# Performance work log

Hardware: AMD Instinct MI355X
Metric: run time of the kernel (lower is better)

## Reference

```python
import jax, jax.numpy as jnp
import numpy as np

SHIFT = 7  # shift_size; pad = 3


def _gn(x, w, b, eps=1e-5):
    # GroupNorm(1, C): normalize over (C,H,W) per sample, affine per channel
    m = jnp.mean(x, axis=(1, 2, 3), keepdims=True)
    v = jnp.var(x, axis=(1, 2, 3), keepdims=True)
    return (x - m) * jax.lax.rsqrt(v + eps) * w[None, :, None, None] + b[None, :, None, None]


def _conv1x1(x, w, b):
    return jnp.einsum('bchw,oc->bohw', x, w) + b[None, :, None, None]


def _gelu(x):
    return jax.nn.gelu(x, approximate=False)


def _shift_h(x, size):
    # CUDA kernel semantics: g = c // ceil(C/size); s = -(g - size//2);
    # out[n,c,h,w] = x[n,c,h+s,w] if in-bounds else 0  (dim=2)
    B, C, H, W = x.shape
    pad = size // 2
    group = -(-C // size)  # ceil
    s = pad - (jnp.arange(C) // group)              # [C], values in [-pad, pad]
    xp = jnp.pad(x, ((0, 0), (0, 0), (pad, pad), (0, 0)))
    idx = jnp.arange(H)[None, :] + s[:, None] + pad  # [C,H], in [0, H+2p-1]
    c = jnp.arange(C)[:, None]
    return xp[:, c, idx, :]


def _shift_w(x, size):
    return _shift_h(x.swapaxes(2, 3), size).swapaxes(2, 3)


def _axial_shift(x, c1w, c1b, n1w, n1b, c21w, c21b, c22w, c22b, n2w, n2b, c3w, c3b):
    x = _gelu(_gn(_conv1x1(x, c1w, c1b), n1w, n1b))
    x_lr = _shift_w(x, SHIFT)
    x_td = _shift_h(x, SHIFT)
    x_lr = _gelu(_conv1x1(x_lr, c21w, c21b))
    x_td = _gelu(_conv1x1(x_td, c22w, c22b))
    x = _gn(x_lr + x_td, n2w, n2b)
    return _conv1x1(x, c3w, c3b)


def setup_inputs() -> dict:
    B, C, H, W = 16, 256, 56, 56
    HID = 4 * C
    key = jax.random.key(0)
    ks = jax.random.split(key, 8)
    wscale = 0.05
    inp = {
        'x': jax.random.normal(ks[0], (B, C, H, W), jnp.float32),
        'n1_w': jnp.ones((C,), jnp.float32), 'n1_b': jnp.zeros((C,), jnp.float32),
        'as_c1_w': jax.random.normal(ks[1], (C, C), jnp.float32) * wscale,
        'as_c1_b': jnp.zeros((C,), jnp.float32),
        'as_n1_w': jnp.ones((C,), jnp.float32), 'as_n1_b': jnp.zeros((C,), jnp.float32),
        'as_c21_w': jax.random.normal(ks[2], (C, C), jnp.float32) * wscale,
        'as_c21_b': jnp.zeros((C,), jnp.float32),
        'as_c22_w': jax.random.normal(ks[3], (C, C), jnp.float32) * wscale,
        'as_c22_b': jnp.zeros((C,), jnp.float32),
        'as_n2_w': jnp.ones((C,), jnp.float32), 'as_n2_b': jnp.zeros((C,), jnp.float32),
        'as_c3_w': jax.random.normal(ks[4], (C, C), jnp.float32) * wscale,
        'as_c3_b': jnp.zeros((C,), jnp.float32),
        'n2_w': jnp.ones((C,), jnp.float32), 'n2_b': jnp.zeros((C,), jnp.float32),
        'fc1_w': jax.random.normal(ks[5], (HID, C), jnp.float32) * wscale,
        'fc1_b': jnp.zeros((HID,), jnp.float32),
        'fc2_w': jax.random.normal(ks[6], (C, HID), jnp.float32) * wscale,
        'fc2_b': jnp.zeros((C,), jnp.float32),
    }
    return inp


def reference(x, n1_w, n1_b, as_c1_w, as_c1_b, as_n1_w, as_n1_b,
              as_c21_w, as_c21_b, as_c22_w, as_c22_b, as_n2_w, as_n2_b,
              as_c3_w, as_c3_b, n2_w, n2_b, fc1_w, fc1_b, fc2_w, fc2_b):
    # AxialShiftedBlock: x = x + AxialShift(norm1(x)); x = x + Mlp(norm2(x))
    h = _gn(x, n1_w, n1_b)
    h = _axial_shift(h, as_c1_w, as_c1_b, as_n1_w, as_n1_b,
                     as_c21_w, as_c21_b, as_c22_w, as_c22_b,
                     as_n2_w, as_n2_b, as_c3_w, as_c3_b)
    x = x + h
    h = _gn(x, n2_w, n2_b)
    h = _gelu(_conv1x1(h, fc1_w, fc1_b))
    h = _conv1x1(h, fc2_w, fc2_b)
    return x + h
```

## Files before the change

kernel.cpp:

```cpp
#include <hip/hip_runtime.h>

typedef __attribute__((ext_vector_type(4))) float f32x4;
typedef __attribute__((ext_vector_type(8))) short bf16x8;
typedef __attribute__((ext_vector_type(4))) unsigned short u16x4;
typedef unsigned short u16;

#define HW 3136
#define NSEG 49
#define NELF 802816.0f
#define EPS 1e-5f

__device__ __forceinline__ short f2bf(float f) {
  union { float f; unsigned u; } v; v.f = f;
  unsigned r = (v.u + 0x7FFFu + ((v.u >> 16) & 1u)) >> 16;
  return (short)r;
}
__device__ __forceinline__ float b2f(u16 u) {
  union { unsigned u; float f; } v; v.u = ((unsigned)u) << 16;
  return v.f;
}
__device__ __forceinline__ float fgelu(float x) {
  float x2 = x * x;
  float u = x * (0.7978845608f + 0.0356774081f * x2);
  float e = __expf(-2.0f * u);
// ... 90 lines not shown
  red[t] = s; red[256 + t] = q;
  __syncthreads();
  for (int off = 128; off > 0; off >>= 1) {
    if (t < off) { red[t] += red[t + off]; red[256 + t] += red[256 + t + off]; }
    __syncthreads();
  }
  if (t == 0) { atomicAdd(&st[n * 2], red[0]); atomicAdd(&st[n * 2 + 1], red[256]); }
}

__global__ void e2_kernel(const u16* __restrict__ y, u16* __restrict__ tb,
                          const float* __restrict__ gw, const float* __restrict__ gb,
                          const float* __restrict__ stats) {
  const size_t NG = (size_t)16 * HW * 32;
  for (size_t g = (size_t)blockIdx.x * blockDim.x + threadIdx.x; g < NG;
       g += (size_t)gridDim.x * blockDim.x) {
    size_t base = g * 8;
    int n = (int)(base / 802816);
    int c0 = (int)(base & 255);
    float sm = stats[n * 2], sq = stats[n * 2 + 1];
    float mn = sm * (1.0f / NELF);
    float rstd = rsqrtf(sq * (1.0f / NELF) - mn * mn + EPS);
    bf16x8 v = *(const bf16x8*)(y + base);
    bf16x8 o;
#pragma unroll
    for (int j = 0; j < 8; ++j) {
      float sc = rstd * gw[c0 + j];
      float sh = gb[c0 + j] - mn * sc;
      o[j] = f2bf(fgelu(b2f((u16)v[j]) * sc + sh));
    }
    *(bf16x8*)(tb + base) = o;
  }
}

#define STG(bsel, ks_) do {                                                              \
    const int k0_ = (ks_) * 32;                                                          \
    if (PRO == 0) {                                                                      \
      gload16(srcB0 + k0_, &lds[16384 + (bsel) * 2048 + wave * 512]);                    \
    } else {                                                                             \
      int c0_ = k0_ + segB * 8;                                                          \
      int g0_ = c0_ / 37;                                                                \
      int js_ = (g0_ + 1) * 37 - c0_;                                                    \
      int s0_ = 3 - g0_;                                                                 \
      if (js_ >= 8) {                                                                    \
        if ((unsigned)(wpB + s0_) < 56u) {                                               \
          int dp_ = (PRO == 1) ? s0_ : 56 * s0_;                                         \
          gload16(actT + (nHW + pB + dp_) * KTOT + segB * 8 + k0_,                       \
                  &lds[16384 + (bsel) * 2048 + wave * 512]);                             \
        } else {                                                                         \
          bf16x8 zz = {0, 0, 0, 0, 0, 0, 0, 0};                                          \
          *(bf16x8*)&lds[16384 + (bsel) * 2048 + t * 8] = zz;                            \
        }                                                                                \
      } else {                                                                           \
        bf16x8 vv;                                                                       \
        _Pragma("unroll") for (int j = 0; j < 8; ++j) {                                  \
          int s_ = s0_ - (j >= js_ ? 1 : 0);                                             \
          int dp_ = (PRO == 1) ? s_ : 56 * s_;                                           \
          int pp_ = pB + dp_; pp_ = pp_ < 0 ? 0 : (pp_ > HW - 1 ? HW - 1 : pp_);         \
          u16 uv = actT[(nHW + pp_) * KTOT + c0_ + j];                                   \
          vv[j] = ((unsigned)(wpB + s_) < 56u) ? (short)uv : (short)0;                   \
        }                                                                                \
        *(bf16x8*)&lds[16384 + (bsel) * 2048 + t * 8] = vv;                              \
      }                                                                                  \
    }                                                                                    \
    gload16(sA0 + k0_, &lds[(bsel) * 8192 + wave * 512]);                                \
    gload16(sA1 + k0_, &lds[(bsel) * 8192 + 2048 + wave * 512]);                         \
    gload16(sA2 + k0_, &lds[(bsel) * 8192 + 4096 + wave * 512]);                         \
    gload16(sA3 + k0_, &lds[(bsel) * 8192 + 6144 + wave * 512]);                         \
  } while (0)

template<int KTOT, int OTOT, int PRO, int EPI>
__global__ __launch_bounds__(256, 3) void gemmS(
    const u16* __restrict__ actT, const u16* __restrict__ wt,
    const float* __restrict__ Sg, const float* __restrict__ Sb,
    const float* __restrict__ stats_in, float* __restrict__ stats_out,
    const u16* __restrict__ residCL, float* __restrict__ out_f32,
    u16* __restrict__ outT)
{
  constexpr int NK = KTOT / 32;
  constexpr bool FOLD = (EPI == 0 || EPI == 1 || EPI == 2);
  __shared__ __align__(16) u16 lds[20480];
  const int t = threadIdx.x;
  const int lane = t & 63, wave = t >> 6;
  const int fr = lane & 15, fq = lane >> 4;
  const int n = blockIdx.x / NSEG;
  const int hw0 = (blockIdx.x % NSEG) * 64;
  const int obase_blk = blockIdx.y * 256;
  const size_t nHW = (size_t)n * HW;

  const int rB = t >> 2;
  const int segB = ((t & 3) - (rB >> 1)) & 3;
  const int pB = hw0 + rB;
  int wpB = 0;
  if (PRO == 1) wpB = pB % 56;
  if (PRO == 2) wpB = pB / 56;
  const u16* srcB0 = actT + (nHW + pB) * KTOT + segB * 8;
  const u16 *sA0, *sA1, *sA2, *sA3;
  {
    int u, r, sg;
    u = t;       r = u >> 2; sg = ((u & 3) - (r >> 1)) & 3; sA0 = wt + (size_t)(obase_blk + r) * KTOT + sg * 8;
    u = t + 256; r = u >> 2; sg = ((u & 3) - (r >> 1)) & 3; sA1 = wt + (size_t)(obase_blk + r) * KTOT + sg * 8;
    u = t + 512; r = u >> 2; sg = ((u & 3) - (r >> 1)) & 3; sA2 = wt + (size_t)(obase_blk + r) * KTOT + sg * 8;
    u = t + 768; r = u >> 2; sg = ((u & 3) - (r >> 1)) & 3; sA3 = wt + (size_t)(obase_blk + r) * KTOT + sg * 8;
  }

  int aU[4], bU[4];
#pragma unroll
  for (int os = 0; os < 4; ++os) { int row = wave * 64 + os * 16 + fr; aU[os] = (4 * row + ((fq + (row >> 1)) & 3)) * 8; }
#pragma unroll
  for (int ps = 0; ps < 4; ++ps) { int row = ps * 16 + fr;             bU[ps] = (4 * row + ((fq + (row >> 1)) & 3)) * 8; }

  float mr = 0.f, rstd = 1.f;
  if (FOLD) {
    float sm = stats_in[n * 2], sq = stats_in[n * 2 + 1];
    float mn = sm * (1.0f / NELF);
    rstd = rsqrtf(sq * (1.0f / NELF) - mn * mn + EPS);
    mr = mn * rstd;
  }

  f32x4 acc[4][4];
#pragma unroll
  for (int a = 0; a < 4; ++a)
#pragma unroll
    for (int b = 0; b < 4; ++b) acc[a][b] = (f32x4){0.f, 0.f, 0.f, 0.f};

  STG(0, 0);
  __syncthreads();
#pragma unroll
  for (int ks = 0; ks < NK; ++ks) {
    const int b = ks & 1;
    if (ks + 1 < NK) STG(b ^ 1, ks + 1);
    bf16x8 afr[4], bfr[4];
#pragma unroll
    for (int os = 0; os < 4; ++os) afr[os] = *(const bf16x8*)&lds[b * 8192 + aU[os]];
#pragma unroll
    for (int ps = 0; ps < 4; ++ps) bfr[ps] = *(const bf16x8*)&lds[16384 + b * 2048 + bU[ps]];
#pragma unroll
    for (int os = 0; os < 4; ++os)
#pragma unroll
      for (int ps = 0; ps < 4; ++ps)
        acc[os][ps] = __builtin_amdgcn_mfma_f32_16x16x32_bf16(afr[os], bfr[ps], acc[os][ps], 0, 0, 0);
    __syncthreads();
  }

  float lsum = 0.f, lsq = 0.f;
  if (EPI != 3) {
#pragma unroll
    for (int os = 0; os < 4; ++os) {
      const int ob = obase_blk + wave * 64 + os * 16 + fq * 4;
      float be[4];
      if (FOLD) {
        float4 g4 = *(const float4*)&Sg[ob];
        float4 s4 = *(const float4*)&Sb[ob];
        be[0] = s4.x - mr * g4.x; be[1] = s4.y - mr * g4.y;
        be[2] = s4.z - mr * g4.z; be[3] = s4.w - mr * g4.w;
      } else {
        float4 s4 = *(const float4*)&Sb[ob];
        be[0] = s4.x; be[1] = s4.y; be[2] = s4.z; be[3] = s4.w;
      }
#pragma unroll
      for (int ps = 0; ps < 4; ++ps) {
        const int pix = ps * 16 + fr;
        u16x4 rv = {0, 0, 0, 0};
        if (EPI == 1 || EPI == 5)
          rv = *(const u16x4*)&residCL[(nHW + hw0 + pix) * 256 + ob];
        u16x4 pk;
#pragma unroll
        for (int j = 0; j < 4; ++j) {
          float v = FOLD ? fmaf(acc[os][ps][j], rstd, be[j]) : (acc[os][ps][j] + be[j]);
          if (EPI == 2 || EPI == 4 || EPI == 5) v = fgelu(v);
          if (EPI == 1 || EPI == 5) v += b2f(rv[j]);
          if (EPI == 0 || EPI == 1 || EPI == 5) { lsum += v; lsq += v * v; }
          pk[j] = (u16)f2bf(v);
        }
        const int qd = wave * 16 + os * 4 + fq;
        const int uq = qd ^ ((pix & 15) << 2);
        *(u16x4*)((char*)lds + pix * 512 + uq * 8) = pk;
      }
    }
    __syncthreads();
    {
      const int p2 = t >> 2;
#pragma unroll
      for (int r = 0; r < 8; ++r) {
        const int oct = (t & 3) + (r << 2);
        const int up = (2 * oct) ^ ((p2 & 15) << 2);
        bf16x8 v = *(const bf16x8*)((char*)lds + p2 * 512 + up * 8);
        *(bf16x8*)&outT[(nHW + hw0 + p2) * OTOT + obase_blk + oct * 8] = v;
      }
    }
  } else {
#pragma unroll
    for (int os = 0; os < 4; ++os) {
      const int ob = wave * 64 + os * 16 + fq * 4;
      float4 b4 = *(const float4*)&Sb[ob];
      float bb[4] = {b4.x, b4.y, b4.z, b4.w};
#pragma unroll
      for (int ps = 0; ps < 4; ++ps) {
        const int pix = ps * 16 + fr;
        u16x4 rv = *(const u16x4*)&residCL[(nHW + hw0 + pix) * 256 + ob];
#pragma unroll
        for (int j = 0; j < 4; ++j)
          out_f32[((size_t)n * 256 + ob + j) * HW + hw0 + pix] = acc[os][ps][j] + bb[j] + b2f(rv[j]);
      }
    }
  }

  if (EPI == 0 || EPI == 1 || EPI == 5) {
    __syncthreads();
    float* red = (float*)lds;
    red[t] = lsum; red[256 + t] = lsq;
    __syncthreads();
    for (int off = 128; off > 0; off >>= 1) {
      if (t < off) { red[t] += red[t + off]; red[256 + t] += red[256 + t + off]; }
      __syncthreads();
    }
    if (t == 0) { atomicAdd(&stats_out[n * 2], red[0]); atomicAdd(&stats_out[n * 2 + 1], red[256]); }
  }
}

extern "C" void kernel_launch(void* const* d_in, const int* in_sizes, int n_in,
                              void* d_out, int out_size, void* d_ws, size_t ws_size,
                              hipStream_t stream) {
  const float* x     = (const float*)d_in[0];
  const float* n1_w  = (const float*)d_in[1];
  const float* n1_b  = (const float*)d_in[2];
  const float* c1_w  = (const float*)d_in[3];
  const float* c1_b  = (const float*)d_in[4];
  const float* an1_w = (const float*)d_in[5];
  const float* an1_b = (const float*)d_in[6];
  const float* c21_w = (const float*)d_in[7];
  const float* c21_b = (const float*)d_in[8];
  const float* c22_w = (const float*)d_in[9];
  const float* c22_b = (const float*)d_in[10];
  const float* an2_w = (const float*)d_in[11];
  const float* an2_b = (const float*)d_in[12];
  const float* c3_w  = (const float*)d_in[13];
  const float* c3_b  = (const float*)d_in[14];
  const float* n2_w  = (const float*)d_in[15];
  const float* n2_b  = (const float*)d_in[16];
  const float* fc1_w = (const float*)d_in[17];
  const float* fc1_b = (const float*)d_in[18];
  const float* fc2_w = (const float*)d_in[19];
  const float* fc2_b = (const float*)d_in[20];

  char* ws = (char*)d_ws;
  float* stats = (float*)ws;
  float* sums  = (float*)(ws + 1024);
  u16* wbuf = (u16*)(ws + 16384);
  u16* wb_c1g  = wbuf;
  u16* wb_c21  = wbuf + 65536;
  u16* wb_c22  = wbuf + 131072;
  u16* wb_c3g  = wbuf + 196608;
  u16* wb_fc1g = wbuf + 262144;
  u16* wb_fc2  = wbuf + 524288;
  const size_t AB = 25690112;
  char* A0 = ws + 1638400;
  u16* xT  = (u16*)(A0);
  u16* yT  = (u16*)(A0 + AB);
  u16* tT  = (u16*)(A0 + 2 * AB);
  u16* zA  = (u16*)(A0 + 3 * AB);
  u16* zT  = (u16*)(A0 + AB);
  u16* x2T = (u16*)(A0 + 4 * AB);
  u16* hid = (u16*)(A0);
  float* out = (float*)d_out;

  hipMemsetAsync(stats, 0, 512, stream);
  wfold_kernel<<<768, 256, 0, stream>>>(c1_w, c21_w, c22_w, c3_w, fc1_w, fc2_w,
                                        n1_w, an2_w, n2_w, wbuf);
  rowsum_kernel<<<6, 256, 0, stream>>>(c1_w, c1_b, n1_w, n1_b, c3_w, c3_b, an2_w, an2_b,
                                       fc1_w, fc1_b, n2_w, n2_b, sums);
  t0_kernel<<<784, 256, 0, stream>>>(x, xT, stats + 0);
  gemmS<256, 256, 0, 0><<<dim3(784, 1), 256, 0, stream>>>(
      xT, wb_c1g, sums, sums + 256, stats + 0, stats + 32, nullptr, nullptr, yT);
  e2_kernel<<<2048, 256, 0, stream>>>(yT, tT, an1_w, an1_b, stats + 32);
  gemmS<256, 256, 1, 4><<<dim3(784, 1), 256, 0, stream>>>(
      tT, wb_c21, nullptr, c21_b, nullptr, nullptr, nullptr, nullptr, zA);
  gemmS<256, 256, 2, 5><<<dim3(784, 1), 256, 0, stream>>>(
      tT, wb_c22, nullptr, c22_b, nullptr, stats + 64, zA, nullptr, zT);
  gemmS<256, 256, 0, 1><<<dim3(784, 1), 256, 0, stream>>>(
      zT, wb_c3g, sums + 512, sums + 768, stats + 64, stats + 96, xT, nullptr, x2T);
  gemmS<256, 1024, 0, 2><<<dim3(784, 4), 256, 0, stream>>>(
      x2T, wb_fc1g, sums + 1024, sums + 2048, stats + 96, nullptr, nullptr, nullptr, hid);
  gemmS<1024, 256, 0, 3><<<dim3(784, 1), 256, 0, stream>>>(
      hid, wb_fc2, nullptr, fc2_b, nullptr, nullptr, x2T, out, nullptr);
}
```

Measured before the change: 317.1 us.

## Retile GEMMs to 256x224 blocks with full-weight LDS residency and 8 waves

```diff
diff --git a/kernel.cpp b/kernel.cpp
--- a/kernel.cpp
+++ b/kernel.cpp
@@ -146,83 +146,124 @@
   }
 }
 
-#define STG(bsel, ks_) do {                                                              \
-    const int k0_ = (ks_) * 32;                                                          \
-    if (PRO == 0) {                                                                      \
-      gload16(srcB0 + k0_, &lds[16384 + (bsel) * 2048 + wave * 512]);                    \
-    } else {                                                                             \
-      int c0_ = k0_ + segB * 8;                                                          \
-      int g0_ = c0_ / 37;                                                                \
-      int js_ = (g0_ + 1) * 37 - c0_;                                                    \
-      int s0_ = 3 - g0_;                                                                 \
-      if (js_ >= 8) {                                                                    \
-        if ((unsigned)(wpB + s0_) < 56u) {                                               \
-          int dp_ = (PRO == 1) ? s0_ : 56 * s0_;                                         \
-          gload16(actT + (nHW + pB + dp_) * KTOT + segB * 8 + k0_,                       \
-                  &lds[16384 + (bsel) * 2048 + wave * 512]);                             \
-        } else {                                                                         \
-          bf16x8 zz = {0, 0, 0, 0, 0, 0, 0, 0};                                          \
-          *(bf16x8*)&lds[16384 + (bsel) * 2048 + t * 8] = zz;                            \
-        }                                                                                \
-      } else {                                                                           \
-        bf16x8 vv;                                                                       \
-        _Pragma("unroll") for (int j = 0; j < 8; ++j) {                                  \
-          int s_ = s0_ - (j >= js_ ? 1 : 0);                                             \
-          int dp_ = (PRO == 1) ? s_ : 56 * s_;                                           \
-          int pp_ = pB + dp_; pp_ = pp_ < 0 ? 0 : (pp_ > HW - 1 ? HW - 1 : pp_);         \
-          u16 uv = actT[(nHW + pp_) * KTOT + c0_ + j];                                   \
-          vv[j] = ((unsigned)(wpB + s_) < 56u) ? (short)uv : (short)0;                   \
-        }                                                                                \
-        *(bf16x8*)&lds[16384 + (bsel) * 2048 + t * 8] = vv;                              \
-      }                                                                                  \
-    }                                                                                    \
-    gload16(sA0 + k0_, &lds[(bsel) * 8192 + wave * 512]);                                \
-    gload16(sA1 + k0_, &lds[(bsel) * 8192 + 2048 + wave * 512]);                         \
-    gload16(sA2 + k0_, &lds[(bsel) * 8192 + 4096 + wave * 512]);                         \
-    gload16(sA3 + k0_, &lds[(bsel) * 8192 + 6144 + wave * 512]);                         \
-  } while (0)
-
-template<int KTOT, int OTOT, int PRO, int EPI>
-__global__ __launch_bounds__(256, 3) void gemmS(
+template<int PRO, int EPI, int OTOT>
+__global__ __launch_bounds__(512, 2) void gemmW(
     const u16* __restrict__ actT, const u16* __restrict__ wt,
     const float* __restrict__ Sg, const float* __restrict__ Sb,
     const float* __restrict__ stats_in, float* __restrict__ stats_out,
-    const u16* __restrict__ residCL, float* __restrict__ out_f32,
-    u16* __restrict__ outT)
+    const u16* __restrict__ residCL, u16* __restrict__ outT)
 {
-  constexpr int NK = KTOT / 32;
   constexpr bool FOLD = (EPI == 0 || EPI == 1 || EPI == 2);
-  __shared__ __align__(16) u16 lds[20480];
+  __shared__ __align__(16) u16 lds[72704];
   const int t = threadIdx.x;
   const int lane = t & 63, wave = t >> 6;
   const int fr = lane & 15, fq = lane >> 4;
-  const int n = blockIdx.x / NSEG;
-  const int hw0 = (blockIdx.x % NSEG) * 64;
-  const int obase_blk = blockIdx.y * 256;
+  const int wo = wave >> 1, wp = wave & 1;
+  const int n = blockIdx.x / 14;
+  const int hw0 = (blockIdx.x % 14) * 224;
+  const int obase = blockIdx.y << 8;
   const size_t nHW = (size_t)n * HW;
 
-  const int rB = t >> 2;
-  const int segB = ((t & 3) - (rB >> 1)) & 3;
-  const int pB = hw0 + rB;
-  int wpB = 0;
-  if (PRO == 1) wpB = pB % 56;
-  if (PRO == 2) wpB = pB / 56;
-  const u16* srcB0 = actT + (nHW + pB) * KTOT + segB * 8;
-  const u16 *sA0, *sA1, *sA2, *sA3;
   {
-    int u, r, sg;
-    u = t;       r = u >> 2; sg = ((u & 3) - (r >> 1)) & 3; sA0 = wt + (size_t)(obase_blk + r) * KTOT + sg * 8;
-    u = t + 256; r = u >> 2; sg = ((u & 3) - (r >> 1)) & 3; sA1 = wt + (size_t)(obase_blk + r) * KTOT + sg * 8;
-    u = t + 512; r = u >> 2; sg = ((u & 3) - (r >> 1)) & 3; sA2 = wt + (size_t)(obase_blk + r) * KTOT + sg * 8;
-    u = t + 768; r = u >> 2; sg = ((u & 3) - (r >> 1)) & 3; sA3 = wt + (size_t)(obase_blk + r) * KTOT + sg * 8;
-  }
-
-  int aU[4], bU[4];
-#pragma unroll
-  for (int os = 0; os < 4; ++os) { int row = wave * 64 + os * 16 + fr; aU[os] = (4 * row + ((fq + (row >> 1)) & 3)) * 8; }
-#pragma unroll
-  for (int ps = 0; ps < 4; ++ps) { int row = ps * 16 + fr;             bU[ps] = (4 * row + ((fq + (row >> 1)) & 3)) * 8; }
-
+    int u0 = t, u1 = t + 512;
+    int r0 = u0 >> 2, sg0 = ((u0 & 3) - (r0 >> 1)) & 3;
+    int r1 = u1 >> 2, sg1 = ((u1 & 3) - (r1 >> 1)) & 3;
+    const u16* w0 = wt + (size_t)(obase + r0) * 256 + sg0 * 8;
+    const u16* w1 = wt + (size_t)(obase + r1) * 256 + sg1 * 8;
+#pragma unroll
+    for (int k = 0; k < 8; ++k) {
+      gload16(w0 + k * 32, &lds[k * 8192 + wave * 512]);
+      gload16(w1 + k * 32, &lds[k * 8192 + 4096 + wave * 512]);
+    }
+  }
+
+  const bool bact = (t < 448);
+  const int brow = t >> 1;
+  const int bp = hw0 + brow;
+  int bwp = 0;
+  if (PRO == 1) bwp = bp % 56;
+  if (PRO == 2) bwp = bp / 56;
+  const int bj0 = (t & 1) * 2;
+  const u16* bsrc = actT + (nHW + bp) * 256;
+
+  auto loadBu = [&](int c0, bf16x8& v) {
+    if (PRO == 0) {
+      v = *(const bf16x8*)(bsrc + c0);
+    } else {
+      int g0 = c0 / 37;
+      int js = (g0 + 1) * 37 - c0;
+      int s0 = 3 - g0;
+      if (js >= 8) {
+        if ((unsigned)(bwp + s0) < 56u) {
+          int dp = (PRO == 1) ? s0 : 56 * s0;
+          v = *(const bf16x8*)(bsrc + dp * 256 + c0);
+        } else {
+          v = (bf16x8){0, 0, 0, 0, 0, 0, 0, 0};
+        }
+      } else {
+#pragma unroll
+        for (int j = 0; j < 8; ++j) {
+          int s = s0 - (j >= js ? 1 : 0);
+          int dp = (PRO == 1) ? s : 56 * s;
+          int pp = bp + dp; pp = pp < 0 ? 0 : (pp > HW - 1 ? HW - 1 : pp);
+          u16 uv = actT[(nHW + pp) * 256 + c0 + j];
+          v[j] = ((unsigned)(bwp + s) < 56u) ? (short)uv : (short)0;
+        }
+      }
+    }
+  };
+
+  int aU[4], bO[7];
+#pragma unroll
+  for (int os = 0; os < 4; ++os) { int row = wo * 64 + os * 16 + fr; aU[os] = (4 * row + ((fq + (row >> 1)) & 3)) * 8; }
+#pragma unroll
+  for (int ps = 0; ps < 7; ++ps) bO[ps] = 65536 + (fq * 224 + wp * 112 + ps * 16 + fr) * 8;
+
+  f32x4 acc[4][7];
+#pragma unroll
+  for (int a = 0; a < 4; ++a)
+#pragma unroll
+    for (int b = 0; b < 7; ++b) acc[a][b] = (f32x4){0.f, 0.f, 0.f, 0.f};
+
+  {
+    bf16x8 v0, v1;
+    if (bact) { loadBu(bj0 * 8, v0); loadBu(bj0 * 8 + 8, v1); }
+    asm volatile("s_waitcnt vmcnt(0)" ::: "memory");
+    if (bact) {
+      *(bf16x8*)&lds[65536 + (bj0 * 224 + brow) * 8] = v0;
+      *(bf16x8*)&lds[65536 + ((bj0 + 1) * 224 + brow) * 8] = v1;
+    }
+  }
+  __syncthreads();
+
+#pragma unroll
+  for (int k = 0; k < 8; ++k) {
+    bf16x8 n0, n1;
+    if (k < 7 && bact) { loadBu((k + 1) * 32 + bj0 * 8, n0); loadBu((k + 1) * 32 + bj0 * 8 + 8, n1); }
+    bf16x8 afr[4], bfr[7];
+#pragma unroll
+    for (int os = 0; os < 4; ++os) afr[os] = *(const bf16x8*)&lds[k * 8192 + aU[os]];
+#pragma unroll
+    for (int ps = 0; ps < 7; ++ps) bfr[ps] = *(const bf16x8*)&lds[bO[ps]];
+#pragma unroll
+    for (int os = 0; os < 4; ++os)
+#pragma unroll
+      for (int ps = 0; ps < 7; ++ps)
+        acc[os][ps] = __builtin_amdgcn_mfma_f32_16x16x32_bf16(afr[os], bfr[ps], acc[os][ps], 0, 0, 0);
+    __builtin_amdgcn_s_barrier();
+    if (k < 7) {
+      if (bact) {
+        *(bf16x8*)&lds[65536 + (bj0 * 224 + brow) * 8] = n0;
+        *(bf16x8*)&lds[65536 + ((bj0 + 1) * 224 + brow) * 8] = n1;
+      }
+      asm volatile("s_waitcnt lgkmcnt(0)" ::: "memory");
+      __builtin_amdgcn_sched_barrier(0);
+      __builtin_amdgcn_s_barrier();
+    }
+  }
+  __syncthreads();
+
+  char* tl = (char*)lds;
   float mr = 0.f, rstd = 1.f;
   if (FOLD) {
     float sm = stats_in[n * 2], sq = stats_in[n * 2 + 1];
@@ -230,105 +271,138 @@
     rstd = rsqrtf(sq * (1.0f / NELF) - mn * mn + EPS);
     mr = mn * rstd;
   }
-
-  f32x4 acc[4][4];
-#pragma unroll
-  for (int a = 0; a < 4; ++a)
-#pragma unroll
-    for (int b = 0; b < 4; ++b) acc[a][b] = (f32x4){0.f, 0.f, 0.f, 0.f};
-
-  STG(0, 0);
-  __syncthreads();
-#pragma unroll
-  for (int ks = 0; ks < NK; ++ks) {
-    const int b = ks & 1;
-    if (ks + 1 < NK) STG(b ^ 1, ks + 1);
-    bf16x8 afr[4], bfr[4];
-#pragma unroll
-    for (int os = 0; os < 4; ++os) afr[os] = *(const bf16x8*)&lds[b * 8192 + aU[os]];
-#pragma unroll
-    for (int ps = 0; ps < 4; ++ps) bfr[ps] = *(const bf16x8*)&lds[16384 + b * 2048 + bU[ps]];
-#pragma unroll
-    for (int os = 0; os < 4; ++os)
-#pragma unroll
-      for (int ps = 0; ps < 4; ++ps)
-        acc[os][ps] = __builtin_amdgcn_mfma_f32_16x16x32_bf16(afr[os], bfr[ps], acc[os][ps], 0, 0, 0);
-    __syncthreads();
-  }
-
   float lsum = 0.f, lsq = 0.f;
-  if (EPI != 3) {
-#pragma unroll
-    for (int os = 0; os < 4; ++os) {
-      const int ob = obase_blk + wave * 64 + os * 16 + fq * 4;
-      float be[4];
-      if (FOLD) {
-        float4 g4 = *(const float4*)&Sg[ob];
-        float4 s4 = *(const float4*)&Sb[ob];
-        be[0] = s4.x - mr * g4.x; be[1] = s4.y - mr * g4.y;
-        be[2] = s4.z - mr * g4.z; be[3] = s4.w - mr * g4.w;
-      } else {
-        float4 s4 = *(const float4*)&Sb[ob];
-        be[0] = s4.x; be[1] = s4.y; be[2] = s4.z; be[3] = s4.w;
+#pragma unroll
+  for (int os = 0; os < 4; ++os) {
+    const int obl = wo * 64 + os * 16 + fq * 4;
+    const int ob = obase + obl;
+    float be[4];
+    if (FOLD) {
+      float4 g4 = *(const float4*)&Sg[ob];
+      float4 s4 = *(const float4*)&Sb[ob];
+      be[0] = s4.x - mr * g4.x; be[1] = s4.y - mr * g4.y;
+      be[2] = s4.z - mr * g4.z; be[3] = s4.w - mr * g4.w;
+    } else {
+      float4 s4 = *(const float4*)&Sb[obl];
+      be[0] = s4.x; be[1] = s4.y; be[2] = s4.z; be[3] = s4.w;
+    }
+#pragma unroll
+    for (int ps = 0; ps < 7; ++ps) {
+      const int pix = wp * 112 + ps * 16 + fr;
+      u16x4 rv = {0, 0, 0, 0};
+      if (EPI == 1 || EPI == 5)
+        rv = *(const u16x4*)&residCL[(nHW + hw0 + pix) * 256 + obl];
+      u16x4 pk;
+#pragma unroll
+      for (int j = 0; j < 4; ++j) {
+        float v = FOLD ? fmaf(acc[os][ps][j], rstd, be[j]) : (acc[os][ps][j] + be[j]);
+        if (EPI == 2 || EPI == 4 || EPI == 5) v = fgelu(v);
+        if (EPI == 1 || EPI == 5) v += b2f(rv[j]);
+        if (EPI == 0 || EPI == 1 || EPI == 5) { lsum += v; lsq += v * v; }
+        pk[j] = (u16)f2bf(v);
       }
-#pragma unroll
-      for (int ps = 0; ps < 4; ++ps) {
-        const int pix = ps * 16 + fr;
-        u16x4 rv = {0, 0, 0, 0};
-        if (EPI == 1 || EPI == 5)
-          rv = *(const u16x4*)&residCL[(nHW + hw0 + pix) * 256 + ob];
-        u16x4 pk;
-#pragma unroll
-        for (int j = 0; j < 4; ++j) {
-          float v = FOLD ? fmaf(acc[os][ps][j], rstd, be[j]) : (acc[os][ps][j] + be[j]);
-          if (EPI == 2 || EPI == 4 || EPI == 5) v = fgelu(v);
-          if (EPI == 1 || EPI == 5) v += b2f(rv[j]);
-          if (EPI == 0 || EPI == 1 || EPI == 5) { lsum += v; lsq += v * v; }
-          pk[j] = (u16)f2bf(v);
-        }
-        const int qd = wave * 16 + os * 4 + fq;
-        const int uq = qd ^ ((pix & 15) << 2);
-        *(u16x4*)((char*)lds + pix * 512 + uq * 8) = pk;
-      }
-    }
-    __syncthreads();
-    {
-      const int p2 = t >> 2;
-#pragma unroll
-      for (int r = 0; r < 8; ++r) {
-        const int oct = (t & 3) + (r << 2);
-        const int up = (2 * oct) ^ ((p2 & 15) << 2);
-        bf16x8 v = *(const bf16x8*)((char*)lds + p2 * 512 + up * 8);
-        *(bf16x8*)&outT[(nHW + hw0 + p2) * OTOT + obase_blk + oct * 8] = v;
-      }
-    }
-  } else {
-#pragma unroll
-    for (int os = 0; os < 4; ++os) {
-      const int ob = wave * 64 + os * 16 + fq * 4;
-      float4 b4 = *(const float4*)&Sb[ob];
-      float bb[4] = {b4.x, b4.y, b4.z, b4.w};
-#pragma unroll
-      for (int ps = 0; ps < 4; ++ps) {
-        const int pix = ps * 16 + fr;
-        u16x4 rv = *(const u16x4*)&residCL[(nHW + hw0 + pix) * 256 + ob];
-#pragma unroll
-        for (int j = 0; j < 4; ++j)
-          out_f32[((size_t)n * 256 + ob + j) * HW + hw0 + pix] = acc[os][ps][j] + bb[j] + b2f(rv[j]);
-      }
-    }
+      const int qd = wo * 16 + os * 4 + fq;
+      const int uq = qd ^ ((pix & 15) << 2);
+      *(u16x4*)(tl + pix * 512 + uq * 8) = pk;
+    }
+  }
+  __syncthreads();
+#pragma unroll
+  for (int r = 0; r < 14; ++r) {
+    int idx = t + r * 512;
+    int pix = idx >> 5, oct = idx & 31;
+    int up = (2 * oct) ^ ((pix & 15) << 2);
+    bf16x8 v = *(const bf16x8*)(tl + pix * 512 + up * 8);
+    *(bf16x8*)&outT[(nHW + hw0 + pix) * OTOT + obase + oct * 8] = v;
   }
 
   if (EPI == 0 || EPI == 1 || EPI == 5) {
     __syncthreads();
     float* red = (float*)lds;
-    red[t] = lsum; red[256 + t] = lsq;
+    red[t] = lsum; red[512 + t] = lsq;
     __syncthreads();
-    for (int off = 128; off > 0; off >>= 1) {
-      if (t < off) { red[t] += red[t + off]; red[256 + t] += red[256 + t + off]; }
+    for (int off = 256; off > 0; off >>= 1) {
+      if (t < off) { red[t] += red[t + off]; red[512 + t] += red[512 + t + off]; }
       __syncthreads();
     }
-    if (t == 0) { atomicAdd(&stats_out[n * 2], red[0]); atomicAdd(&stats_out[n * 2 + 1], red[256]); }
+    if (t == 0) { atomicAdd(&stats_out[n * 2], red[0]); atomicAdd(&stats_out[n * 2 + 1], red[512]); }
+  }
+}
+
+__global__ __launch_bounds__(512, 2) void gemmF(
+    const u16* __restrict__ hidT, const u16* __restrict__ wt,
+    const float* __restrict__ bias, const u16* __restrict__ residCL,
+    float* __restrict__ out_f32)
+{
+  __shared__ __align__(16) u16 lds[30720];
+  const int t = threadIdx.x;
+  const int lane = t & 63, wave = t >> 6;
+  const int fr = lane & 15, fq = lane >> 4;
+  const int wo = wave >> 1, wp = wave & 1;
+  const int n = blockIdx.x / 14;
+  const int hw0 = (blockIdx.x % 14) * 224;
+  const size_t nHW = (size_t)n * HW;
+
+  int u0 = t, u1 = t + 512;
+  int r0 = u0 >> 2, sg0 = ((u0 & 3) - (r0 >> 1)) & 3;
+  int r1 = u1 >> 2, sg1 = ((u1 & 3) - (r1 >> 1)) & 3;
+  const u16* wA0 = wt + (size_t)r0 * 1024 + sg0 * 8;
+  const u16* wA1 = wt + (size_t)r1 * 1024 + sg1 * 8;
+  const int c1 = (2 * wave) % 14, c2 = (2 * wave + 1) % 14;
+  const int ub1 = c1 * 64 + lane, ub2 = c2 * 64 + lane;
+  const u16* hb1 = hidT + (nHW + hw0 + ub1 % 224) * 1024 + (ub1 / 224) * 8;
+  const u16* hb2 = hidT + (nHW + hw0 + ub2 % 224) * 1024 + (ub2 / 224) * 8;
+
+  auto stgf = [&](int bs, int k0) {
+    gload16(wA0 + k0, &lds[bs * 8192 + wave * 512]);
+    gload16(wA1 + k0, &lds[bs * 8192 + 4096 + wave * 512]);
+    gload16(hb1 + k0, &lds[16384 + bs * 7168 + c1 * 512]);
+    gload16(hb2 + k0, &lds[16384 + bs * 7168 + c2 * 512]);
+  };
+
+  int aU[4], bO[7];
+#pragma unroll
+  for (int os = 0; os < 4; ++os) { int row = wo * 64 + os * 16 + fr; aU[os] = (4 * row + ((fq + (row >> 1)) & 3)) * 8; }
+#pragma unroll
+  for (int ps = 0; ps < 7; ++ps) bO[ps] = 16384 + (fq * 224 + wp * 112 + ps * 16 + fr) * 8;
+
+  f32x4 acc[4][7];
+#pragma unroll
+  for (int a = 0; a < 4; ++a)
+#pragma unroll
+    for (int b = 0; b < 7; ++b) acc[a][b] = (f32x4){0.f, 0.f, 0.f, 0.f};
+
+  stgf(0, 0);
+  __syncthreads();
+  for (int ks = 0; ks < 32; ++ks) {
+    const int bs = ks & 1;
+    if (ks < 31) stgf(bs ^ 1, (ks + 1) * 32);
+    bf16x8 afr[4], bfr[7];
+#pragma unroll
+    for (int os = 0; os < 4; ++os) afr[os] = *(const bf16x8*)&lds[bs * 8192 + aU[os]];
+#pragma unroll
+    for (int ps = 0; ps < 7; ++ps) bfr[ps] = *(const bf16x8*)&lds[bs * 7168 + bO[ps]];
+#pragma unroll
+    for (int os = 0; os < 4; ++os)
+#pragma unroll
+      for (int ps = 0; ps < 7; ++ps)
+        acc[os][ps] = __builtin_amdgcn_mfma_f32_16x16x32_bf16(afr[os], bfr[ps], acc[os][ps], 0, 0, 0);
+    __syncthreads();
+  }
+
+#pragma unroll
+  for (int os = 0; os < 4; ++os) {
+    const int ob = wo * 64 + os * 16 + fq * 4;
+    float4 b4 = *(const float4*)&bias[ob];
+    float bb[4] = {b4.x, b4.y, b4.z, b4.w};
+#pragma unroll
+    for (int ps = 0; ps < 7; ++ps) {
+      const int pix = wp * 112 + ps * 16 + fr;
+      u16x4 rv = *(const u16x4*)&residCL[(nHW + hw0 + pix) * 256 + ob];
+#pragma unroll
+      for (int j = 0; j < 4; ++j)
+        out_f32[((size_t)n * 256 + ob + j) * HW + hw0 + pix] = acc[os][ps][j] + bb[j] + b2f(rv[j]);
+    }
   }
 }
 
@@ -384,17 +458,16 @@
   rowsum_kernel<<<6, 256, 0, stream>>>(c1_w, c1_b, n1_w, n1_b, c3_w, c3_b, an2_w, an2_b,
                                        fc1_w, fc1_b, n2_w, n2_b, sums);
   t0_kernel<<<784, 256, 0, stream>>>(x, xT, stats + 0);
-  gemmS<256, 256, 0, 0><<<dim3(784, 1), 256, 0, stream>>>(
-      xT, wb_c1g, sums, sums + 256, stats + 0, stats + 32, nullptr, nullptr, yT);
+  gemmW<0, 0, 256><<<dim3(224, 1), 512, 0, stream>>>(
+      xT, wb_c1g, sums, sums + 256, stats + 0, stats + 32, nullptr, yT);
   e2_kernel<<<2048, 256, 0, stream>>>(yT, tT, an1_w, an1_b, stats + 32);
-  gemmS<256, 256, 1, 4><<<dim3(784, 1), 256, 0, stream>>>(
-      tT, wb_c21, nullptr, c21_b, nullptr, nullptr, nullptr, nullptr, zA);
-  gemmS<256, 256, 2, 5><<<dim3(784, 1), 256, 0, stream>>>(
-      tT, wb_c22, nullptr, c22_b, nullptr, stats + 64, zA, nullptr, zT);
-  gemmS<256, 256, 0, 1><<<dim3(784, 1), 256, 0, stream>>>(
-      zT, wb_c3g, sums + 512, sums + 768, stats + 64, stats + 96, xT, nullptr, x2T);
-  gemmS<256, 1024, 0, 2><<<dim3(784, 4), 256, 0, stream>>>(
-      x2T, wb_fc1g, sums + 1024, sums + 2048, stats + 96, nullptr, nullptr, nullptr, hid);
-  gemmS<1024, 256, 0, 3><<<dim3(784, 1), 256, 0, stream>>>(
-      hid, wb_fc2, nullptr, fc2_b, nullptr, nullptr, x2T, out, nullptr);
-}
+  gemmW<1, 4, 256><<<dim3(224, 1), 512, 0, stream>>>(
+      tT, wb_c21, nullptr, c21_b, nullptr, nullptr, nullptr, zA);
+  gemmW<2, 5, 256><<<dim3(224, 1), 512, 0, stream>>>(
+      tT, wb_c22, nullptr, c22_b, nullptr, stats + 64, zA, zT);
+  gemmW<0, 1, 256><<<dim3(224, 1), 512, 0, stream>>>(
+      zT, wb_c3g, sums + 512, sums + 768, stats + 64, stats + 96, xT, x2T);
+  gemmW<0, 2, 1024><<<dim3(224, 4), 512, 0, stream>>>(
+      x2T, wb_fc1g, sums + 1024, sums + 2048, stats + 96, nullptr, nullptr, hid);
+  gemmF<<<224, 512, 0, stream>>>(hid, wb_fc2, fc2_b, x2T, out);
+}
```

Result: faster. 289.9 us (-8.6%).

## Retile GEMMs to 128x128 square tiles and fuse both shift convolutions

Applied to the files above, without the earlier changes.

```diff
diff --git a/kernel.cpp b/kernel.cpp
--- a/kernel.cpp
+++ b/kernel.cpp
@@ -146,90 +146,41 @@
   }
 }
 
-#define STG(bsel, ks_) do {                                                              \
-    const int k0_ = (ks_) * 32;                                                          \
-    if (PRO == 0) {                                                                      \
-      gload16(srcB0 + k0_, &lds[16384 + (bsel) * 2048 + wave * 512]);                    \
-    } else {                                                                             \
-      int c0_ = k0_ + segB * 8;                                                          \
-      int g0_ = c0_ / 37;                                                                \
-      int js_ = (g0_ + 1) * 37 - c0_;                                                    \
-      int s0_ = 3 - g0_;                                                                 \
-      if (js_ >= 8) {                                                                    \
-        if ((unsigned)(wpB + s0_) < 56u) {                                               \
-          int dp_ = (PRO == 1) ? s0_ : 56 * s0_;                                         \
-          gload16(actT + (nHW + pB + dp_) * KTOT + segB * 8 + k0_,                       \
-                  &lds[16384 + (bsel) * 2048 + wave * 512]);                             \
-        } else {                                                                         \
-          bf16x8 zz = {0, 0, 0, 0, 0, 0, 0, 0};                                          \
-          *(bf16x8*)&lds[16384 + (bsel) * 2048 + t * 8] = zz;                            \
-        }                                                                                \
-      } else {                                                                           \
-        bf16x8 vv;                                                                       \
-        _Pragma("unroll") for (int j = 0; j < 8; ++j) {                                  \
-          int s_ = s0_ - (j >= js_ ? 1 : 0);                                             \
-          int dp_ = (PRO == 1) ? s_ : 56 * s_;                                           \
-          int pp_ = pB + dp_; pp_ = pp_ < 0 ? 0 : (pp_ > HW - 1 ? HW - 1 : pp_);         \
-          u16 uv = actT[(nHW + pp_) * KTOT + c0_ + j];                                   \
-          vv[j] = ((unsigned)(wpB + s_) < 56u) ? (short)uv : (short)0;                   \
-        }                                                                                \
-        *(bf16x8*)&lds[16384 + (bsel) * 2048 + t * 8] = vv;                              \
-      }                                                                                  \
-    }                                                                                    \
-    gload16(sA0 + k0_, &lds[(bsel) * 8192 + wave * 512]);                                \
-    gload16(sA1 + k0_, &lds[(bsel) * 8192 + 2048 + wave * 512]);                         \
-    gload16(sA2 + k0_, &lds[(bsel) * 8192 + 4096 + wave * 512]);                         \
-    gload16(sA3 + k0_, &lds[(bsel) * 8192 + 6144 + wave * 512]);                         \
+#define SQ_STAGE(par, ks) do {                                          \
+    gload16(srcA0 + (ks) * 32, &lds[(par) * 4096 + t * 8]);             \
+    gload16(srcA1 + (ks) * 32, &lds[(par) * 4096 + 2048 + t * 8]);      \
+    gload16(srcB0 + (ks) * 32, &lds[8192 + (par) * 4096 + t * 8]);      \
+    gload16(srcB1 + (ks) * 32, &lds[8192 + (par) * 4096 + 2048 + t * 8]); \
   } while (0)
 
-template<int KTOT, int OTOT, int PRO, int EPI>
-__global__ __launch_bounds__(256, 3) void gemmS(
+template<int KTOT, int OTOT, int EPI>
+__global__ __launch_bounds__(256, 3) void sq128(
     const u16* __restrict__ actT, const u16* __restrict__ wt,
     const float* __restrict__ Sg, const float* __restrict__ Sb,
     const float* __restrict__ stats_in, float* __restrict__ stats_out,
     const u16* __restrict__ residCL, float* __restrict__ out_f32,
-    u16* __restrict__ outT)
+    u16* __restrict__ outCL)
 {
   constexpr int NK = KTOT / 32;
-  constexpr bool FOLD = (EPI == 0 || EPI == 1 || EPI == 2);
-  __shared__ __align__(16) u16 lds[20480];
+  __shared__ __align__(16) u16 lds[16384];
   const int t = threadIdx.x;
   const int lane = t & 63, wave = t >> 6;
   const int fr = lane & 15, fq = lane >> 4;
-  const int n = blockIdx.x / NSEG;
-  const int hw0 = (blockIdx.x % NSEG) * 64;
-  const int obase_blk = blockIdx.y * 256;
-  const size_t nHW = (size_t)n * HW;
-
-  const int rB = t >> 2;
-  const int segB = ((t & 3) - (rB >> 1)) & 3;
-  const int pB = hw0 + rB;
-  int wpB = 0;
-  if (PRO == 1) wpB = pB % 56;
-  if (PRO == 2) wpB = pB / 56;
-  const u16* srcB0 = actT + (nHW + pB) * KTOT + segB * 8;
-  const u16 *sA0, *sA1, *sA2, *sA3;
-  {
-    int u, r, sg;
-    u = t;       r = u >> 2; sg = ((u & 3) - (r >> 1)) & 3; sA0 = wt + (size_t)(obase_blk + r) * KTOT + sg * 8;
-    u = t + 256; r = u >> 2; sg = ((u & 3) - (r >> 1)) & 3; sA1 = wt + (size_t)(obase_blk + r) * KTOT + sg * 8;
-    u = t + 512; r = u >> 2; sg = ((u & 3) - (r >> 1)) & 3; sA2 = wt + (size_t)(obase_blk + r) * KTOT + sg * 8;
-    u = t + 768; r = u >> 2; sg = ((u & 3) - (r >> 1)) & 3; sA3 = wt + (size_t)(obase_blk + r) * KTOT + sg * 8;
-  }
+  const int wo = wave >> 1, wp = wave & 1;
+  const int obase = blockIdx.x * 128;
+  const int gp0 = blockIdx.y * 128;
+
+  const int r0 = t >> 2, sg0 = ((t & 3) - (r0 >> 1)) & 3;
+  const u16* srcA0 = wt + (size_t)(obase + r0) * KTOT + sg0 * 8;
+  const u16* srcA1 = wt + (size_t)(obase + 64 + r0) * KTOT + sg0 * 8;
+  const u16* srcB0 = actT + (size_t)(gp0 + r0) * KTOT + sg0 * 8;
+  const u16* srcB1 = actT + (size_t)(gp0 + 64 + r0) * KTOT + sg0 * 8;
 
   int aU[4], bU[4];
 #pragma unroll
-  for (int os = 0; os < 4; ++os) { int row = wave * 64 + os * 16 + fr; aU[os] = (4 * row + ((fq + (row >> 1)) & 3)) * 8; }
-#pragma unroll
-  for (int ps = 0; ps < 4; ++ps) { int row = ps * 16 + fr;             bU[ps] = (4 * row + ((fq + (row >> 1)) & 3)) * 8; }
-
-  float mr = 0.f, rstd = 1.f;
-  if (FOLD) {
-    float sm = stats_in[n * 2], sq = stats_in[n * 2 + 1];
-    float mn = sm * (1.0f / NELF);
-    rstd = rsqrtf(sq * (1.0f / NELF) - mn * mn + EPS);
-    mr = mn * rstd;
-  }
+  for (int os = 0; os < 4; ++os) { int row = wo * 64 + os * 16 + fr; aU[os] = (4 * row + ((fq + (row >> 1)) & 3)) * 8; }
+#pragma unroll
+  for (int ps = 0; ps < 4; ++ps) { int row = wp * 64 + ps * 16 + fr; bU[ps] = 8192 + (4 * row + ((fq + (row >> 1)) & 3)) * 8; }
 
   f32x4 acc[4][4];
 #pragma unroll
@@ -237,17 +188,16 @@
 #pragma unroll
     for (int b = 0; b < 4; ++b) acc[a][b] = (f32x4){0.f, 0.f, 0.f, 0.f};
 
-  STG(0, 0);
-  __syncthreads();
-#pragma unroll
+  SQ_STAGE(0, 0);
+  __syncthreads();
   for (int ks = 0; ks < NK; ++ks) {
-    const int b = ks & 1;
-    if (ks + 1 < NK) STG(b ^ 1, ks + 1);
+    const int par = ks & 1;
+    if (ks + 1 < NK) SQ_STAGE(par ^ 1, ks + 1);
     bf16x8 afr[4], bfr[4];
 #pragma unroll
-    for (int os = 0; os < 4; ++os) afr[os] = *(const bf16x8*)&lds[b * 8192 + aU[os]];
-#pragma unroll
-    for (int ps = 0; ps < 4; ++ps) bfr[ps] = *(const bf16x8*)&lds[16384 + b * 2048 + bU[ps]];
+    for (int os = 0; os < 4; ++os) afr[os] = *(const bf16x8*)&lds[par * 4096 + aU[os]];
+#pragma unroll
+    for (int ps = 0; ps < 4; ++ps) bfr[ps] = *(const bf16x8*)&lds[par * 4096 + bU[ps]];
 #pragma unroll
     for (int os = 0; os < 4; ++os)
 #pragma unroll
@@ -256,79 +206,248 @@
     __syncthreads();
   }
 
-  float lsum = 0.f, lsq = 0.f;
+  const int n0 = gp0 / HW;
+  const int bnd = (n0 + 1) * HW;
+  const int n1 = (n0 < 15) ? n0 + 1 : n0;
+
   if (EPI != 3) {
+    float rstd0 = 1.f, mr0 = 0.f, rstd1 = 1.f, mr1 = 0.f;
+    {
+      float sm = stats_in[n0 * 2], sq = stats_in[n0 * 2 + 1];
+      float mn = sm * (1.0f / NELF);
+      rstd0 = rsqrtf(sq * (1.0f / NELF) - mn * mn + EPS); mr0 = mn * rstd0;
+      float sm1 = stats_in[n1 * 2], sq1 = stats_in[n1 * 2 + 1];
+      float mn1 = sm1 * (1.0f / NELF);
+      rstd1 = rsqrtf(sq1 * (1.0f / NELF) - mn1 * mn1 + EPS); mr1 = mn1 * rstd1;
+    }
+    char* tl = (char*)lds;
 #pragma unroll
     for (int os = 0; os < 4; ++os) {
-      const int ob = obase_blk + wave * 64 + os * 16 + fq * 4;
-      float be[4];
-      if (FOLD) {
-        float4 g4 = *(const float4*)&Sg[ob];
-        float4 s4 = *(const float4*)&Sb[ob];
-        be[0] = s4.x - mr * g4.x; be[1] = s4.y - mr * g4.y;
-        be[2] = s4.z - mr * g4.z; be[3] = s4.w - mr * g4.w;
-      } else {
-        float4 s4 = *(const float4*)&Sb[ob];
-        be[0] = s4.x; be[1] = s4.y; be[2] = s4.z; be[3] = s4.w;
-      }
+      const int chl = wo * 64 + os * 16 + fq * 4;
+      const int ob = obase + chl;
+      float4 g4 = *(const float4*)&Sg[ob];
+      float4 s4 = *(const float4*)&Sb[ob];
+      float be0[4] = {s4.x - mr0 * g4.x, s4.y - mr0 * g4.y, s4.z - mr0 * g4.z, s4.w - mr0 * g4.w};
+      float be1[4] = {s4.x - mr1 * g4.x, s4.y - mr1 * g4.y, s4.z - mr1 * g4.z, s4.w - mr1 * g4.w};
+      const int q8 = chl >> 2;
 #pragma unroll
       for (int ps = 0; ps < 4; ++ps) {
-        const int pix = ps * 16 + fr;
+        const int lp = wp * 64 + ps * 16 + fr;
+        const int gpix = gp0 + lp;
+        const bool hi = (gpix >= bnd);
+        const float rs = hi ? rstd1 : rstd0;
         u16x4 rv = {0, 0, 0, 0};
-        if (EPI == 1 || EPI == 5)
-          rv = *(const u16x4*)&residCL[(nHW + hw0 + pix) * 256 + ob];
+        if (EPI == 1) rv = *(const u16x4*)&residCL[(size_t)gpix * 256 + ob];
         u16x4 pk;
 #pragma unroll
         for (int j = 0; j < 4; ++j) {
-          float v = FOLD ? fmaf(acc[os][ps][j], rstd, be[j]) : (acc[os][ps][j] + be[j]);
-          if (EPI == 2 || EPI == 4 || EPI == 5) v = fgelu(v);
-          if (EPI == 1 || EPI == 5) v += b2f(rv[j]);
-          if (EPI == 0 || EPI == 1 || EPI == 5) { lsum += v; lsq += v * v; }
+          float v = fmaf(acc[os][ps][j], rs, hi ? be1[j] : be0[j]);
+          if (EPI == 1) v += b2f(rv[j]);
+          if (EPI == 2) v = fgelu(v);
           pk[j] = (u16)f2bf(v);
         }
-        const int qd = wave * 16 + os * 4 + fq;
-        const int uq = qd ^ ((pix & 15) << 2);
-        *(u16x4*)((char*)lds + pix * 512 + uq * 8) = pk;
+        *(u16x4*)(tl + lp * 256 + ((q8 ^ ((lp & 7) << 1)) & 31) * 8) = pk;
       }
     }
     __syncthreads();
-    {
-      const int p2 = t >> 2;
-#pragma unroll
-      for (int r = 0; r < 8; ++r) {
-        const int oct = (t & 3) + (r << 2);
-        const int up = (2 * oct) ^ ((p2 & 15) << 2);
-        bf16x8 v = *(const bf16x8*)((char*)lds + p2 * 512 + up * 8);
-        *(bf16x8*)&outT[(nHW + hw0 + p2) * OTOT + obase_blk + oct * 8] = v;
+    float ls0 = 0.f, lq0 = 0.f, ls1 = 0.f, lq1 = 0.f;
+#pragma unroll
+    for (int r = 0; r < 8; ++r) {
+      const int idx = r * 256 + t;
+      const int p = idx >> 4, o8 = idx & 15;
+      bf16x8 v = *(const bf16x8*)(tl + p * 256 + (((2 * o8) ^ ((p & 7) << 1)) & 31) * 8);
+      *(bf16x8*)&outCL[(size_t)(gp0 + p) * OTOT + obase + o8 * 8] = v;
+      if (EPI == 0 || EPI == 1) {
+        const bool hi = (gp0 + p >= bnd);
+        float s = 0.f, q = 0.f;
+#pragma unroll
+        for (int j = 0; j < 8; ++j) { float f = b2f((u16)v[j]); s += f; q += f * f; }
+        if (hi) { ls1 += s; lq1 += q; } else { ls0 += s; lq0 += q; }
       }
     }
+    if (EPI == 0 || EPI == 1) {
+      __syncthreads();
+      float* red = (float*)lds;
+      red[t] = ls0; red[256 + t] = lq0; red[512 + t] = ls1; red[768 + t] = lq1;
+      __syncthreads();
+      for (int off = 128; off > 0; off >>= 1) {
+        if (t < off) {
+          red[t] += red[t + off]; red[256 + t] += red[256 + t + off];
+          red[512 + t] += red[512 + t + off]; red[768 + t] += red[768 + t + off];
+        }
+        __syncthreads();
+      }
+      if (t == 0) {
+        atomicAdd(&stats_out[n0 * 2], red[0]); atomicAdd(&stats_out[n0 * 2 + 1], red[256]);
+        atomicAdd(&stats_out[n1 * 2], red[512]); atomicAdd(&stats_out[n1 * 2 + 1], red[768]);
+      }
+    }
   } else {
 #pragma unroll
     for (int os = 0; os < 4; ++os) {
-      const int ob = wave * 64 + os * 16 + fq * 4;
+      const int ob = obase + wo * 64 + os * 16 + fq * 4;
       float4 b4 = *(const float4*)&Sb[ob];
       float bb[4] = {b4.x, b4.y, b4.z, b4.w};
 #pragma unroll
       for (int ps = 0; ps < 4; ++ps) {
-        const int pix = ps * 16 + fr;
-        u16x4 rv = *(const u16x4*)&residCL[(nHW + hw0 + pix) * 256 + ob];
+        const int gpix = gp0 + wp * 64 + ps * 16 + fr;
+        const bool hi = (gpix >= bnd);
+        const int n = hi ? n0 + 1 : n0;
+        const int hw = gpix - n * HW;
+        u16x4 rv = *(const u16x4*)&residCL[(size_t)gpix * 256 + ob];
 #pragma unroll
         for (int j = 0; j < 4; ++j)
-          out_f32[((size_t)n * 256 + ob + j) * HW + hw0 + pix] = acc[os][ps][j] + bb[j] + b2f(rv[j]);
+          out_f32[((size_t)n * 256 + ob + j) * HW + hw] = acc[os][ps][j] + bb[j] + b2f(rv[j]);
       }
     }
   }
-
-  if (EPI == 0 || EPI == 1 || EPI == 5) {
+}
+
+__global__ __launch_bounds__(512, 2) void dual6(
+    const u16* __restrict__ tT, const u16* __restrict__ w21, const u16* __restrict__ w22,
+    const float* __restrict__ b21, const float* __restrict__ b22,
+    float* __restrict__ stats_out, u16* __restrict__ zT)
+{
+  __shared__ __align__(16) u16 lds[24576];
+  const int t = threadIdx.x;
+  const int lane = t & 63, wave = t >> 6;
+  const int fr = lane & 15, fq = lane >> 4;
+  const int conv = wave >> 2, wq = wave & 3;
+  const int obase = blockIdx.x * 64;
+  const int gp0 = blockIdx.y * 128;
+
+  const int uA = t & 255, rA = uA >> 2, sgA = ((uA & 3) - (rA >> 1)) & 3;
+  const u16* srcA = (t < 256 ? w21 : w22) + (size_t)(obase + rA) * 256 + sgA * 8;
+  const int dstA = ((t < 256) ? 0 : 2048) + uA * 8;
+
+  const int gp_ = t >> 2;
+  const int oct_ = ((t & 3) - (gp_ >> 1)) & 3;
+  const int gpix = gp0 + gp_;
+  const int ng = gpix / HW, hwg = gpix - ng * HW;
+  const int wc = hwg % 56, hc = hwg / 56;
+  const size_t rowb = (size_t)ng * HW;
+
+  bf16x8 gA0, gA1, gB0, gB1;
+  auto gatherIssue = [&](int ks) {
+    int c0 = ks * 32 + oct_ * 8;
+    int g0 = c0 / 37;
+    int s0 = 3 - g0;
+    int pa0 = hwg + s0;            pa0 = pa0 < 0 ? 0 : (pa0 > HW - 1 ? HW - 1 : pa0);
+    int pa1 = hwg + s0 - 1;        pa1 = pa1 < 0 ? 0 : (pa1 > HW - 1 ? HW - 1 : pa1);
+    int pb0 = hwg + 56 * s0;       pb0 = pb0 < 0 ? 0 : (pb0 > HW - 1 ? HW - 1 : pb0);
+    int pb1 = hwg + 56 * (s0 - 1); pb1 = pb1 < 0 ? 0 : (pb1 > HW - 1 ? HW - 1 : pb1);
+    gA0 = *(const bf16x8*)(tT + (rowb + pa0) * 256 + c0);
+    gA1 = *(const bf16x8*)(tT + (rowb + pa1) * 256 + c0);
+    gB0 = *(const bf16x8*)(tT + (rowb + pb0) * 256 + c0);
+    gB1 = *(const bf16x8*)(tT + (rowb + pb1) * 256 + c0);
+  };
+  auto gatherWrite = [&](int par, int ks) {
+    int c0 = ks * 32 + oct_ * 8;
+    int g0 = c0 / 37;
+    int s0 = 3 - g0;
+    int js = (g0 + 1) * 37 - c0; if (js > 8) js = 8;
+    bool a0 = (unsigned)(wc + s0) < 56u, a1 = (unsigned)(wc + s0 - 1) < 56u;
+    bool b0 = (unsigned)(hc + s0) < 56u, b1 = (unsigned)(hc + s0 - 1) < 56u;
+    bf16x8 va, vb;
+#pragma unroll
+    for (int j = 0; j < 8; ++j) {
+      bool lo = j < js;
+      va[j] = lo ? (a0 ? gA0[j] : (short)0) : (a1 ? gA1[j] : (short)0);
+      vb[j] = lo ? (b0 ? gB0[j] : (short)0) : (b1 ? gB1[j] : (short)0);
+    }
+    *(bf16x8*)&lds[8192 + par * 8192 + t * 8] = va;
+    *(bf16x8*)&lds[8192 + par * 8192 + 4096 + t * 8] = vb;
+  };
+
+  int aU[4], bU[2];
+#pragma unroll
+  for (int os = 0; os < 4; ++os) { int row = os * 16 + fr; aU[os] = conv * 2048 + (4 * row + ((fq + (row >> 1)) & 3)) * 8; }
+#pragma unroll
+  for (int ps = 0; ps < 2; ++ps) { int row = wq * 32 + ps * 16 + fr; bU[ps] = 8192 + conv * 4096 + (4 * row + ((fq + (row >> 1)) & 3)) * 8; }
+
+  f32x4 acc[4][2];
+#pragma unroll
+  for (int a = 0; a < 4; ++a)
+#pragma unroll
+    for (int b = 0; b < 2; ++b) acc[a][b] = (f32x4){0.f, 0.f, 0.f, 0.f};
+
+  gatherIssue(0);
+  gload16(srcA, &lds[dstA]);
+  gatherWrite(0, 0);
+  __syncthreads();
+
+#pragma unroll
+  for (int ks = 0; ks < 8; ++ks) {
+    const int par = ks & 1;
+    if (ks < 7) { gatherIssue(ks + 1); gload16(srcA + (ks + 1) * 32, &lds[(par ^ 1) * 4096 + dstA]); }
+    bf16x8 afr[4], bfr[2];
+#pragma unroll
+    for (int os = 0; os < 4; ++os) afr[os] = *(const bf16x8*)&lds[par * 4096 + aU[os]];
+#pragma unroll
+    for (int ps = 0; ps < 2; ++ps) bfr[ps] = *(const bf16x8*)&lds[par * 8192 + bU[ps]];
+#pragma unroll
+    for (int os = 0; os < 4; ++os)
+#pragma unroll
+      for (int ps = 0; ps < 2; ++ps)
+        acc[os][ps] = __builtin_amdgcn_mfma_f32_16x16x32_bf16(afr[os], bfr[ps], acc[os][ps], 0, 0, 0);
+    if (ks < 7) gatherWrite(par ^ 1, ks + 1);
     __syncthreads();
-    float* red = (float*)lds;
-    red[t] = lsum; red[256 + t] = lsq;
+  }
+
+  char* tl = (char*)lds;
+  const float* bias = conv ? b22 : b21;
+#pragma unroll
+  for (int os = 0; os < 4; ++os) {
+    const int chl = os * 16 + fq * 4;
+    float4 b4 = *(const float4*)&bias[obase + chl];
+    float bb[4] = {b4.x, b4.y, b4.z, b4.w};
+    const int q8 = chl >> 2;
+#pragma unroll
+    for (int ps = 0; ps < 2; ++ps) {
+      const int p = wq * 32 + ps * 16 + fr;
+      u16x4 pk;
+#pragma unroll
+      for (int j = 0; j < 4; ++j) pk[j] = (u16)f2bf(fgelu(acc[os][ps][j] + bb[j]));
+      *(u16x4*)(tl + conv * 16384 + p * 128 + ((q8 ^ ((p & 7) << 1)) & 15) * 8) = pk;
+    }
+  }
+  __syncthreads();
+  const int n0 = gp0 / HW;
+  const int bnd = (n0 + 1) * HW;
+  const int n1 = (n0 < 15) ? n0 + 1 : n0;
+  float ls0 = 0.f, lq0 = 0.f, ls1 = 0.f, lq1 = 0.f;
+#pragma unroll
+  for (int r = 0; r < 2; ++r) {
+    const int idx = r * 512 + t;
+    const int p = idx >> 3, o8 = idx & 7;
+    const int uq = (((2 * o8) ^ ((p & 7) << 1)) & 15) * 8;
+    bf16x8 vA = *(const bf16x8*)(tl + p * 128 + uq);
+    bf16x8 vB = *(const bf16x8*)(tl + 16384 + p * 128 + uq);
+    bf16x8 o;
+    float s = 0.f, q = 0.f;
+#pragma unroll
+    for (int j = 0; j < 8; ++j) {
+      float z = b2f((u16)vA[j]) + b2f((u16)vB[j]);
+      s += z; q += z * z;
+      o[j] = f2bf(z);
+    }
+    *(bf16x8*)&zT[(size_t)(gp0 + p) * 256 + obase + o8 * 8] = o;
+    if (gp0 + p >= bnd) { ls1 += s; lq1 += q; } else { ls0 += s; lq0 += q; }
+  }
+  __syncthreads();
+  float* red = (float*)lds;
+  red[t] = ls0; red[512 + t] = lq0; red[1024 + t] = ls1; red[1536 + t] = lq1;
+  __syncthreads();
+  for (int off = 256; off > 0; off >>= 1) {
+    if (t < off) {
+      red[t] += red[t + off]; red[512 + t] += red[512 + t + off];
+      red[1024 + t] += red[1024 + t + off]; red[1536 + t] += red[1536 + t + off];
+    }
     __syncthreads();
-    for (int off = 128; off > 0; off >>= 1) {
-      if (t < off) { red[t] += red[t + off]; red[256 + t] += red[256 + t + off]; }
-      __syncthreads();
-    }
-    if (t == 0) { atomicAdd(&stats_out[n * 2], red[0]); atomicAdd(&stats_out[n * 2 + 1], red[256]); }
+  }
+  if (t == 0) {
+    atomicAdd(&stats_out[n0 * 2], red[0]); atomicAdd(&stats_out[n0 * 2 + 1], red[512]);
+    atomicAdd(&stats_out[n1 * 2], red[1024]); atomicAdd(&stats_out[n1 * 2 + 1], red[1536]);
   }
 }
 
@@ -372,8 +491,7 @@
   u16* xT  = (u16*)(A0);
   u16* yT  = (u16*)(A0 + AB);
   u16* tT  = (u16*)(A0 + 2 * AB);
-  u16* zA  = (u16*)(A0 + 3 * AB);
-  u16* zT  = (u16*)(A0 + AB);
+  u16* zT  = (u16*)(A0 + 3 * AB);
   u16* x2T = (u16*)(A0 + 4 * AB);
   u16* hid = (u16*)(A0);
   float* out = (float*)d_out;
@@ -384,17 +502,14 @@
   rowsum_kernel<<<6, 256, 0, stream>>>(c1_w, c1_b, n1_w, n1_b, c3_w, c3_b, an2_w, an2_b,
                                        fc1_w, fc1_b, n2_w, n2_b, sums);
   t0_kernel<<<784, 256, 0, stream>>>(x, xT, stats + 0);
-  gemmS<256, 256, 0, 0><<<dim3(784, 1), 256, 0, stream>>>(
+  sq128<256, 256, 0><<<dim3(2, 392), 256, 0, stream>>>(
       xT, wb_c1g, sums, sums + 256, stats + 0, stats + 32, nullptr, nullptr, yT);
   e2_kernel<<<2048, 256, 0, stream>>>(yT, tT, an1_w, an1_b, stats + 32);
-  gemmS<256, 256, 1, 4><<<dim3(784, 1), 256, 0, stream>>>(
-      tT, wb_c21, nullptr, c21_b, nullptr, nullptr, nullptr, nullptr, zA);
-  gemmS<256, 256, 2, 5><<<dim3(784, 1), 256, 0, stream>>>(
-      tT, wb_c22, nullptr, c22_b, nullptr, stats + 64, zA, nullptr, zT);
-  gemmS<256, 256, 0, 1><<<dim3(784, 1), 256, 0, stream>>>(
+  dual6<<<dim3(4, 392), 512, 0, stream>>>(tT, wb_c21, wb_c22, c21_b, c22_b, stats + 64, zT);
+  sq128<256, 256, 1><<<dim3(2, 392), 256, 0, stream>>>(
       zT, wb_c3g, sums + 512, sums + 768, stats + 64, stats + 96, xT, nullptr, x2T);
-  gemmS<256, 1024, 0, 2><<<dim3(784, 4), 256, 0, stream>>>(
+  sq128<256, 1024, 2><<<dim3(8, 392), 256, 0, stream>>>(
       x2T, wb_fc1g, sums + 1024, sums + 2048, stats + 96, nullptr, nullptr, nullptr, hid);
-  gemmS<1024, 256, 0, 3><<<dim3(784, 1), 256, 0, stream>>>(
+  sq128<1024, 256, 3><<<dim3(2, 392), 256, 0, stream>>>(
       hid, wb_fc2, nullptr, fc2_b, nullptr, nullptr, x2T, out, nullptr);
 }
```

New measurement: 382.7 us. 20.7% more time.
